# Kernel optimization log

Measured on AMD Instinct MI355X. Metric: run time of the kernel, lower is better.

Reference implementation:

```python
import jax, jax.numpy as jnp
import numpy as np

N = 50000        # nodes
E = 800000       # edges (avg degree 16)
F_IN, F_HID, F_OUT = 128, 256, 256
G = 64           # graphs in batch
NEG_SLOPE_ATT = 0.2   # GATConv attention leaky relu
NEG_SLOPE_ACT = 0.01  # nn.LeakyReLU default


def setup_inputs() -> dict:
    key = jax.random.key(0)
    ks = jax.random.split(key, 12)
    x = jax.random.normal(ks[0], (N, F_IN), dtype=jnp.float32)
    edge_index = jax.random.randint(ks[1], (2, E), 0, N, dtype=jnp.int64)
    batch = jnp.sort(jax.random.randint(ks[2], (N,), 0, G, dtype=jnp.int64))
    def glorot(k, shape):
        fan = sum(shape)
        s = jnp.sqrt(6.0 / fan).astype(jnp.float32)
        return jax.random.uniform(k, shape, jnp.float32, -s, s)
    W1 = glorot(ks[3], (F_IN, F_HID))
    a_s1 = glorot(ks[4], (F_HID,))
    a_d1 = glorot(ks[5], (F_HID,))
    b1 = jnp.zeros((F_HID,), jnp.float32)
    W2 = glorot(ks[6], (F_HID, F_OUT))
    a_s2 = glorot(ks[7], (F_OUT,))
    a_d2 = glorot(ks[8], (F_OUT,))
    b2 = jnp.zeros((F_OUT,), jnp.float32)
    return dict(x=x, edge_index=edge_index, batch=batch,
                W1=W1, a_s1=a_s1, a_d1=a_d1, b1=b1,
                W2=W2, a_s2=a_s2, a_d2=a_d2, b2=b2)


def gat_conv(x, src, dst, W, a_s, a_d, b):
    """Single-head PyG GATConv (self-loops already appended to src/dst)."""
    n = x.shape[0]
    h = x @ W                                   # [N, D]
    alpha_src = h @ a_s                         # [N]
    alpha_dst = h @ a_d                         # [N]
    e = jax.nn.leaky_relu(alpha_src[src] + alpha_dst[dst], NEG_SLOPE_ATT)  # [E+N]
    m = jax.ops.segment_max(e, dst, num_segments=n)
    p = jnp.exp(e - jax.lax.stop_gradient(m)[dst])
    denom = jax.ops.segment_sum(p, dst, num_segments=n)
    alpha = p / denom[dst]                      # softmax over incoming edges
    out = jax.ops.segment_sum(h[src] * alpha[:, None], dst, num_segments=n)
    return out + b


def reference(x, edge_index, batch, W1, a_s1, a_d1, b1, W2, a_s2, a_d2, b2):
    n = x.shape[0]
    loops = jnp.arange(n, dtype=edge_index.dtype)   # GATConv add_self_loops=True
    src = jnp.concatenate([edge_index[0], loops])
    dst = jnp.concatenate([edge_index[1], loops])
    h = gat_conv(x, src, dst, W1, a_s1, a_d1, b1)
    h = jax.nn.leaky_relu(h, NEG_SLOPE_ACT)         # dropout is identity in eval
    node_emb = gat_conv(h, src, dst, W2, a_s2, a_d2, b2)
    graph_emb = jax.ops.segment_sum(node_emb, batch, num_segments=G)
    return node_emb, graph_emb
```

## Files before the change

kernel.cpp:

```cpp
#include <hip/hip_runtime.h>
#include <math.h>

#define NN 50000
#define NE 800000
#define F_IN 128
#define F_HID 256
#define NG 64
#define NPART 8
#define CSR_CHUNKS 128
#define SLOTS 64

typedef __bf16 bf16x8 __attribute__((ext_vector_type(8)));
typedef float f32x4 __attribute__((ext_vector_type(4)));
typedef float f32x2 __attribute__((ext_vector_type(2)));
typedef unsigned short u16x8 __attribute__((ext_vector_type(8)));

static __device__ __forceinline__ unsigned short f2bf(float f) {
    union { float f; unsigned u; } v; v.f = f;
    unsigned r = v.u + 0x7fff + ((v.u >> 16) & 1);
    return (unsigned short)(r >> 16);
}
static __device__ __forceinline__ float bf2f(unsigned short u) {
    union { unsigned u; float f; } v; v.u = ((unsigned)u) << 16;
    return v.f;
}
static __device__ __forceinline__ f32x2 bf2x2(unsigned u) {
    union { unsigned u; float f; } lo, hi;
    lo.u = u << 16;
    hi.u = u & 0xffff0000u;
    f32x2 r; r[0] = lo.f; r[1] = hi.f;
    return r;
}

template <int K, bool AF32, bool ZG>
__global__ __launch_bounds__(256)
void gemm_mfma(const void* __restrict__ Ap, const ushort* __restrict__ Wt,
               ushort* __restrict__ C16, const float* __restrict__ a_s,
               const float* __restrict__ a_d, float* __restrict__ as_out,
               float* __restrict__ ad_out, float* __restrict__ gemb, int M) {
    const ushort* A16 = (const ushort*)Ap;
    const float* A32 = (const float*)Ap;
    __shared__ ushort As[64 * 72];
    __shared__ ushort Bs[256 * 72];
    __shared__ float dps[4][64];
    __shared__ float dpd[4][64];
    const int t = threadIdx.x;
    if (ZG && blockIdx.x < NG) gemb[(size_t)blockIdx.x * 256 + t] = 0.f;
    const int bm = blockIdx.x * 64;
    const int wv = t >> 6, lane = t & 63;
    const int wn = wv * 64;
    const int lrow = lane & 15, quad = lane >> 4;
    const int ar = t >> 2;
    const int ac = (t & 3) << 4;

    f32x4 acc[4][4];
    #pragma unroll
    for (int i = 0; i < 4; ++i)
        #pragma unroll
        for (int j = 0; j < 4; ++j)
            #pragma unroll
            for (int r = 0; r < 4; ++r) acc[i][j][r] = 0.f;

    const int r0 = bm + ar;

    auto load_a = [&](int k0, u16x8& a0, u16x8& a1) {
        a0 = (u16x8)(0); a1 = (u16x8)(0);
        if (r0 < M) {
            if (AF32) {
                const float* p = A32 + (size_t)r0 * K + k0 + ac;
                float4 f0 = *(const float4*)p, f1 = *(const float4*)(p + 4);
                float4 f2 = *(const float4*)(p + 8), f3 = *(const float4*)(p + 12);
                a0[0]=f2bf(f0.x); a0[1]=f2bf(f0.y); a0[2]=f2bf(f0.z); a0[3]=f2bf(f0.w);
                a0[4]=f2bf(f1.x); a0[5]=f2bf(f1.y); a0[6]=f2bf(f1.z); a0[7]=f2bf(f1.w);
                a1[0]=f2bf(f2.x); a1[1]=f2bf(f2.y); a1[2]=f2bf(f2.z); a1[3]=f2bf(f2.w);
                a1[4]=f2bf(f3.x); a1[5]=f2bf(f3.y); a1[6]=f2bf(f3.z); a1[7]=f2bf(f3.w);
            } else {
                const ushort* p = A16 + (size_t)r0 * K + k0 + ac;
                a0 = *(const u16x8*)p;
                a1 = *(const u16x8*)(p + 8);
            }
        }
    };
    auto load_b = [&](int k0, u16x8* b) {
        const ushort* p = Wt + (size_t)t * K + k0;
        #pragma unroll
        for (int j = 0; j < 8; ++j) b[j] = *(const u16x8*)(p + j * 8);
    };

    u16x8 a0, a1, b[8];
    load_a(0, a0, a1);
    load_b(0, b);

    for (int k0 = 0; k0 < K; k0 += 64) {
        __syncthreads();
        *(u16x8*)(As + ar * 72 + ac) = a0;
        *(u16x8*)(As + ar * 72 + ac + 8) = a1;
        #pragma unroll
        for (int j = 0; j < 8; ++j) *(u16x8*)(Bs + t * 72 + j * 8) = b[j];
        __syncthreads();
        bool more = (k0 + 64) < K;
        u16x8 na0, na1, nb[8];
        if (more) {
            load_a(k0 + 64, na0, na1);
            load_b(k0 + 64, nb);
        }
        #pragma unroll
        for (int s = 0; s < 2; ++s) {
            bf16x8 af[4], bf_[4];
            #pragma unroll
            for (int i = 0; i < 4; ++i)
                af[i] = *(const bf16x8*)(As + (i * 16 + lrow) * 72 + s * 32 + quad * 8);
            #pragma unroll
            for (int j = 0; j < 4; ++j)
                bf_[j] = *(const bf16x8*)(Bs + (wn + j * 16 + lrow) * 72 + s * 32 + quad * 8);
            #pragma unroll
            for (int i = 0; i < 4; ++i)
                #pragma unroll
                for (int j = 0; j < 4; ++j)
                    acc[i][j] = __builtin_amdgcn_mfma_f32_16x16x32_bf16(
                        af[i], bf_[j], acc[i][j], 0, 0, 0);
        }
        if (more) {
            a0 = na0; a1 = na1;
            #pragma unroll
            for (int j = 0; j < 8; ++j) b[j] = nb[j];
        }
    }
    float asf[4], adf[4];
    #pragma unroll
    for (int j = 0; j < 4; ++j) {
        asf[j] = a_s[wn + j * 16 + lrow];
        adf[j] = a_d[wn + j * 16 + lrow];
    }
    #pragma unroll
    for (int i = 0; i < 4; ++i) {
        #pragma unroll
        for (int r = 0; r < 4; ++r) {
            float ps = 0.f, pd = 0.f;
            #pragma unroll
            for (int j = 0; j < 4; ++j) {
                ps += acc[i][j][r] * asf[j];
                pd += acc[i][j][r] * adf[j];
            }
            #pragma unroll
            for (int off = 8; off; off >>= 1) {
                ps += __shfl_xor(ps, off);
                pd += __shfl_xor(pd, off);
            }
            if (lrow == 0) {
                dps[wv][i * 16 + quad * 4 + r] = ps;
                dpd[wv][i * 16 + quad * 4 + r] = pd;
            }
        }
    }
    __syncthreads();
    if (t < 64 && bm + t < M) {
        as_out[bm + t] = dps[0][t] + dps[1][t] + dps[2][t] + dps[3][t];
        ad_out[bm + t] = dpd[0][t] + dpd[1][t] + dpd[2][t] + dpd[3][t];
    }
    #pragma unroll
    for (int i = 0; i < 4; ++i) {
        int gm0 = bm + i * 16 + quad * 4;
        #pragma unroll
        for (int j = 0; j < 4; ++j) {
            int gn = wn + j * 16 + lrow;
            #pragma unroll
            for (int r = 0; r < 4; ++r)
                if (gm0 + r < M) C16[(size_t)(gm0 + r) * 256 + gn] = f2bf(acc[i][j][r]);
        }
    }
}

__global__ void cvt_wts(const float* __restrict__ W1, ushort* __restrict__ Wt1,
                        const float* __restrict__ W2, ushort* __restrict__ Wt2,
                        int* __restrict__ cursor) {
    int idx = blockIdx.x * blockDim.x + threadIdx.x;
    if (idx < NN) cursor[idx] = 0;
    if (idx < 256 * F_IN) {
        int n = idx / F_IN, k = idx - n * F_IN;
        Wt1[idx] = f2bf(W1[(size_t)k * 256 + n]);
    } else if (idx < 256 * F_IN + 256 * F_HID) {
        int i2 = idx - 256 * F_IN;
        int n = i2 / F_HID, k = i2 - n * F_HID;
        Wt2[i2] = f2bf(W2[(size_t)k * 256 + n]);
    }
}

__global__ __launch_bounds__(256)
void scatter_part(const int* __restrict__ src, const int* __restrict__ dst,
                  int* __restrict__ cursor, int* __restrict__ src_sorted,
                  int E, int n) {
    const int p = blockIdx.x & (NPART - 1);
    const int c = blockIdx.x >> 3;
    const int T = E + n;
    const int chunk = (T + CSR_CHUNKS - 1) / CSR_CHUNKS;
    const int i0 = c * chunk;
    const int i1 = min(i0 + chunk, T);
    for (int i = i0 + (int)threadIdx.x; i < i1; i += 256) {
        int d = (i < E) ? dst[i] : (i - E);
        int pd = (d * NPART) / NN;
        if (pd == p) {
            int s = (i < E) ? src[i] : d;
            int pos = atomicAdd(&cursor[d], 1);
            if (pos < SLOTS) src_sorted[(size_t)d * SLOTS + pos] = s;
        }
    }
}

template <bool ACT, bool BF16OUT, bool POOL>
__global__ __launch_bounds__(256)
void agg_kernel(const ushort* __restrict__ h, const float* __restrict__ as,
                const float* __restrict__ ad, const int* __restrict__ degs,
                const int* __restrict__ src_sorted, const float* __restrict__ bias,
                float* __restrict__ out, ushort* __restrict__ out16,
                const int* __restrict__ batch, float* __restrict__ gemb, int n) {
    const int hw = threadIdx.x >> 5;
    const int lane = threadIdx.x & 63;
    const int hl = lane & 31;
    const int base = lane & 32;
    const int node = blockIdx.x * 8 + hw;
    __shared__ float vbuf[8][256];
    __shared__ int gids[8];

    const bool valid = node < n;
    int deg = 0, start = 0;
    float adn = 0.f;
    if (valid) {
        deg = min(degs[node], SLOTS);
        start = node * SLOTS;
        adn = ad[node];
    }

    int s_lane = 0;
    float e_lane = -INFINITY;
    if (valid && hl < deg) {
        s_lane = src_sorted[start + hl];
        float e = as[s_lane] + adn;
        e_lane = e > 0.f ? e : 0.2f * e;
    }
    float m = e_lane;
    for (int j = 32 + hl; j < deg; j += 32) {
        int s = src_sorted[start + j];
        float e = as[s] + adn;
        e = e > 0.f ? e : 0.2f * e;
        m = fmaxf(m, e);
    }
    #pragma unroll
    for (int off = 16; off; off >>= 1) m = fmaxf(m, __shfl_xor(m, off));
    float p_lane = __expf(e_lane - m);
    float denom = p_lane;
    for (int j = 32 + hl; j < deg; j += 32) {
        int s = src_sorted[start + j];
        float e = as[s] + adn;
        e = e > 0.f ? e : 0.2f * e;
        denom += __expf(e - m);
    }
    #pragma unroll
    for (int off = 16; off; off >>= 1) denom += __shfl_xor(denom, off);
    float inv = valid ? (1.f / denom) : 0.f;
    p_lane *= inv;

    const ushort* hrow = h + hl * 8;
    f32x2 acc2[4];
    #pragma unroll
    for (int q = 0; q < 4; ++q) { acc2[q][0] = 0.f; acc2[q][1] = 0.f; }
    const int degc = min(deg, 32);
    for (int j0 = 0; j0 < degc; j0 += 4) {
        float wa = __shfl(p_lane, base | j0);       int sa = __shfl(s_lane, base | j0);
        float wb = __shfl(p_lane, base | (j0 + 1)); int sb = __shfl(s_lane, base | (j0 + 1));
        float wc = __shfl(p_lane, base | (j0 + 2)); int sc = __shfl(s_lane, base | (j0 + 2));
        float wd = __shfl(p_lane, base | (j0 + 3)); int sd = __shfl(s_lane, base | (j0 + 3));
        wb = (j0 + 1 < degc) ? wb : 0.f;
        wc = (j0 + 2 < degc) ? wc : 0.f;
        wd = (j0 + 3 < degc) ? wd : 0.f;
        uint4 ra = *(const uint4*)(hrow + (size_t)sa * 256);
        uint4 rb = *(const uint4*)(hrow + (size_t)sb * 256);
        uint4 rc = *(const uint4*)(hrow + (size_t)sc * 256);
        uint4 rd = *(const uint4*)(hrow + (size_t)sd * 256);
        f32x2 wa2; wa2[0] = wa; wa2[1] = wa;
        f32x2 wb2; wb2[0] = wb; wb2[1] = wb;
        f32x2 wc2; wc2[0] = wc; wc2[1] = wc;
        f32x2 wd2; wd2[0] = wd; wd2[1] = wd;
        acc2[0] += wa2 * bf2x2(ra.x); acc2[1] += wa2 * bf2x2(ra.y);
        acc2[2] += wa2 * bf2x2(ra.z); acc2[3] += wa2 * bf2x2(ra.w);
        acc2[0] += wb2 * bf2x2(rb.x); acc2[1] += wb2 * bf2x2(rb.y);
        acc2[2] += wb2 * bf2x2(rb.z); acc2[3] += wb2 * bf2x2(rb.w);
        acc2[0] += wc2 * bf2x2(rc.x); acc2[1] += wc2 * bf2x2(rc.y);
        acc2[2] += wc2 * bf2x2(rc.z); acc2[3] += wc2 * bf2x2(rc.w);
        acc2[0] += wd2 * bf2x2(rd.x); acc2[1] += wd2 * bf2x2(rd.y);
        acc2[2] += wd2 * bf2x2(rd.z); acc2[3] += wd2 * bf2x2(rd.w);
    }
    if (deg > 32) {
        for (int j = 32; j < deg; ++j) {
            int s = src_sorted[start + j];
            float e = as[s] + adn;
            e = e > 0.f ? e : 0.2f * e;
            float w = __expf(e - m) * inv;
            uint4 r = *(const uint4*)(hrow + (size_t)s * 256);
            f32x2 w2; w2[0] = w; w2[1] = w;
            acc2[0] += w2 * bf2x2(r.x); acc2[1] += w2 * bf2x2(r.y);
            acc2[2] += w2 * bf2x2(r.z); acc2[3] += w2 * bf2x2(r.w);
        }
    }
    const float4* b4 = (const float4*)bias;
    float4 b0 = b4[hl * 2], b1 = b4[hl * 2 + 1];
    float v[8];
    v[0] = acc2[0][0] + b0.x; v[1] = acc2[0][1] + b0.y;
    v[2] = acc2[1][0] + b0.z; v[3] = acc2[1][1] + b0.w;
    v[4] = acc2[2][0] + b1.x; v[5] = acc2[2][1] + b1.y;
    v[6] = acc2[3][0] + b1.z; v[7] = acc2[3][1] + b1.w;
    if (ACT) {
        #pragma unroll
        for (int k = 0; k < 8; ++k) v[k] = v[k] > 0.f ? v[k] : 0.01f * v[k];
    }
    if (valid) {
        if (BF16OUT) {
            u16x8 o;
            #pragma unroll
            for (int k = 0; k < 8; ++k) o[k] = f2bf(v[k]);
            *(u16x8*)(out16 + (size_t)node * 256 + hl * 8) = o;
        } else {
            float4 o0 = make_float4(v[0], v[1], v[2], v[3]);
            float4 o1 = make_float4(v[4], v[5], v[6], v[7]);
            float4* op = (float4*)(out + (size_t)node * 256);
            op[hl * 2] = o0;
            op[hl * 2 + 1] = o1;
        }
    }
    if (POOL) {
        *(float4*)&vbuf[hw][hl * 8]     = make_float4(v[0], v[1], v[2], v[3]);
        *(float4*)&vbuf[hw][hl * 8 + 4] = make_float4(v[4], v[5], v[6], v[7]);
        if (hl == 0) gids[hw] = valid ? batch[node] : -1;
        __syncthreads();
        const int t = threadIdx.x;
        float acc = 0.f;
        int cur = gids[0];
        #pragma unroll
        for (int i = 0; i < 8; ++i) {
            int g = gids[i];
            if (g < 0) break;
            if (g != cur) {
                atomicAdd(&gemb[(size_t)cur * 256 + t], acc);
                acc = 0.f; cur = g;
            }
            acc += vbuf[i][t];
        }
        if (cur >= 0) atomicAdd(&gemb[(size_t)cur * 256 + t], acc);
    }
}

static inline char* align_up(char* p, size_t a) {
    return (char*)(((uintptr_t)p + a - 1) & ~(uintptr_t)(a - 1));
}

extern "C" void kernel_launch(void* const* d_in, const int* in_sizes, int n_in,
                              void* d_out, int out_size, void* d_ws, size_t ws_size,
                              hipStream_t stream) {
    const float* x     = (const float*)d_in[0];
    const int* eidx    = (const int*)d_in[1];
    const int* batch   = (const int*)d_in[2];
    const float* W1    = (const float*)d_in[3];
    const float* a_s1  = (const float*)d_in[4];
    const float* a_d1  = (const float*)d_in[5];
    const float* b1    = (const float*)d_in[6];
    const float* W2    = (const float*)d_in[7];
    const float* a_s2  = (const float*)d_in[8];
    const float* a_d2  = (const float*)d_in[9];
    const float* b2    = (const float*)d_in[10];

    float* node_emb  = (float*)d_out;
    float* graph_emb = node_emb + (size_t)NN * 256;

    char* ws = (char*)d_ws;
    ushort* h16  = (ushort*)ws;  ws += (size_t)NN * 256 * sizeof(ushort);
    ws = align_up(ws, 256);
    ushort* z16  = (ushort*)ws;  ws += (size_t)NN * 256 * sizeof(ushort);
    ws = align_up(ws, 256);
    ushort* wt1  = (ushort*)ws;  ws += (size_t)256 * F_IN * sizeof(ushort);
    ws = align_up(ws, 256);
    ushort* wt2  = (ushort*)ws;  ws += (size_t)256 * F_HID * sizeof(ushort);
    ws = align_up(ws, 256);
    float* as_buf = (float*)ws;  ws += (size_t)NN * sizeof(float);
    float* ad_buf = (float*)ws;  ws += (size_t)NN * sizeof(float);
    int* cursor   = (int*)ws;    ws += (size_t)NN * sizeof(int);
    ws = align_up(ws, 256);
    int* src_sorted = (int*)ws;  ws += (size_t)NN * SLOTS * sizeof(int);

    const int* e_src = eidx;
    const int* e_dst = eidx + NE;

    int gemm_blocks = (NN + 63) / 64;
    int agg_blocks = (NN + 7) / 8;

    cvt_wts<<<(256 * (F_IN + F_HID) + 255) / 256, 256, 0, stream>>>(W1, wt1, W2, wt2, cursor);

    scatter_part<<<NPART * CSR_CHUNKS, 256, 0, stream>>>(e_src, e_dst, cursor, src_sorted, NE, NN);

    gemm_mfma<F_IN, true, false><<<gemm_blocks, 256, 0, stream>>>(
        x, wt1, h16, a_s1, a_d1, as_buf, ad_buf, nullptr, NN);
    agg_kernel<true, true, false><<<agg_blocks, 256, 0, stream>>>(
        h16, as_buf, ad_buf, cursor, src_sorted, b1, nullptr, z16, nullptr, nullptr, NN);

    gemm_mfma<F_HID, false, true><<<gemm_blocks, 256, 0, stream>>>(
        z16, wt2, h16, a_s2, a_d2, as_buf, ad_buf, graph_emb, NN);
    agg_kernel<false, false, true><<<agg_blocks, 256, 0, stream>>>(
        h16, as_buf, ad_buf, cursor, src_sorted, b2, node_emb, nullptr, batch, graph_emb, NN);
}
```

Measured before the change: 316.2 us.

## Quantize node features to int8 with per-row scales for aggregation gathers

The GEMM epilogue now computes a per-row absmax, stores a scale per node, and writes the transformed features as int8 instead of bf16. The aggregation kernels gather 8-byte int8 rows and fold the scale into the attention weight, halving gather traffic over the roughly 850K edges. The cost is an extra reduction and barrier in the GEMM epilogue, byte-granular scattered stores, more integer-to-float conversion work per gathered element, and reduced numerical precision that may exceed tolerance.

```diff
diff --git a/kernel.cpp b/kernel.cpp
--- a/kernel.cpp
+++ b/kernel.cpp
@@ -12,7 +12,6 @@
 
 typedef __bf16 bf16x8 __attribute__((ext_vector_type(8)));
 typedef float f32x4 __attribute__((ext_vector_type(4)));
-typedef float f32x2 __attribute__((ext_vector_type(2)));
 typedef unsigned short u16x8 __attribute__((ext_vector_type(8)));
 
 static __device__ __forceinline__ unsigned short f2bf(float f) {
@@ -20,30 +19,30 @@
     unsigned r = v.u + 0x7fff + ((v.u >> 16) & 1);
     return (unsigned short)(r >> 16);
 }
-static __device__ __forceinline__ float bf2f(unsigned short u) {
-    union { unsigned u; float f; } v; v.u = ((unsigned)u) << 16;
-    return v.f;
-}
-static __device__ __forceinline__ f32x2 bf2x2(unsigned u) {
-    union { unsigned u; float f; } lo, hi;
-    lo.u = u << 16;
-    hi.u = u & 0xffff0000u;
-    f32x2 r; r[0] = lo.f; r[1] = hi.f;
-    return r;
+static __device__ __forceinline__ void i8fma(float* acc8, unsigned lo, unsigned hi, float w) {
+    #pragma unroll
+    for (int k = 0; k < 4; ++k)
+        acc8[k]     += w * (float)(int)(signed char)(lo >> (k * 8));
+    #pragma unroll
+    for (int k = 0; k < 4; ++k)
+        acc8[k + 4] += w * (float)(int)(signed char)(hi >> (k * 8));
 }
 
 template <int K, bool AF32, bool ZG>
 __global__ __launch_bounds__(256)
 void gemm_mfma(const void* __restrict__ Ap, const ushort* __restrict__ Wt,
-               ushort* __restrict__ C16, const float* __restrict__ a_s,
-               const float* __restrict__ a_d, float* __restrict__ as_out,
-               float* __restrict__ ad_out, float* __restrict__ gemb, int M) {
+               signed char* __restrict__ C8, float* __restrict__ scales,
+               const float* __restrict__ a_s, const float* __restrict__ a_d,
+               float* __restrict__ as_out, float* __restrict__ ad_out,
+               float* __restrict__ gemb, int M) {
     const ushort* A16 = (const ushort*)Ap;
     const float* A32 = (const float*)Ap;
     __shared__ ushort As[64 * 72];
     __shared__ ushort Bs[256 * 72];
     __shared__ float dps[4][64];
     __shared__ float dpd[4][64];
+    __shared__ float rmx[4][64];
+    __shared__ float rinvs[64];
     const int t = threadIdx.x;
     if (ZG && blockIdx.x < NG) gemb[(size_t)blockIdx.x * 256 + t] = 0.f;
     const int bm = blockIdx.x * 64;
@@ -136,37 +135,53 @@
     for (int i = 0; i < 4; ++i) {
         #pragma unroll
         for (int r = 0; r < 4; ++r) {
-            float ps = 0.f, pd = 0.f;
+            float ps = 0.f, pd = 0.f, mx = 0.f;
             #pragma unroll
             for (int j = 0; j < 4; ++j) {
                 ps += acc[i][j][r] * asf[j];
                 pd += acc[i][j][r] * adf[j];
+                mx = fmaxf(mx, fabsf(acc[i][j][r]));
             }
             #pragma unroll
             for (int off = 8; off; off >>= 1) {
                 ps += __shfl_xor(ps, off);
                 pd += __shfl_xor(pd, off);
+                mx = fmaxf(mx, __shfl_xor(mx, off));
             }
             if (lrow == 0) {
                 dps[wv][i * 16 + quad * 4 + r] = ps;
                 dpd[wv][i * 16 + quad * 4 + r] = pd;
+                rmx[wv][i * 16 + quad * 4 + r] = mx;
             }
         }
     }
     __syncthreads();
-    if (t < 64 && bm + t < M) {
-        as_out[bm + t] = dps[0][t] + dps[1][t] + dps[2][t] + dps[3][t];
-        ad_out[bm + t] = dpd[0][t] + dpd[1][t] + dpd[2][t] + dpd[3][t];
-    }
+    if (t < 64) {
+        float mx = fmaxf(fmaxf(rmx[0][t], rmx[1][t]), fmaxf(rmx[2][t], rmx[3][t]));
+        rinvs[t] = mx > 0.f ? 127.f / mx : 0.f;
+        if (bm + t < M) {
+            scales[bm + t] = mx * (1.f / 127.f);
+            as_out[bm + t] = dps[0][t] + dps[1][t] + dps[2][t] + dps[3][t];
+            ad_out[bm + t] = dpd[0][t] + dpd[1][t] + dpd[2][t] + dpd[3][t];
+        }
+    }
+    __syncthreads();
     #pragma unroll
     for (int i = 0; i < 4; ++i) {
-        int gm0 = bm + i * 16 + quad * 4;
-        #pragma unroll
-        for (int j = 0; j < 4; ++j) {
-            int gn = wn + j * 16 + lrow;
-            #pragma unroll
-            for (int r = 0; r < 4; ++r)
-                if (gm0 + r < M) C16[(size_t)(gm0 + r) * 256 + gn] = f2bf(acc[i][j][r]);
+        #pragma unroll
+        for (int r = 0; r < 4; ++r) {
+            int rl = i * 16 + quad * 4 + r;
+            int gm = bm + rl;
+            if (gm < M) {
+                float rinv = rinvs[rl];
+                #pragma unroll
+                for (int j = 0; j < 4; ++j) {
+                    int gn = wn + j * 16 + lrow;
+                    int qi = __float2int_rn(acc[i][j][r] * rinv);
+                    qi = max(-127, min(127, qi));
+                    C8[(size_t)gm * 256 + gn] = (signed char)qi;
+                }
+            }
         }
     }
 }
@@ -209,11 +224,12 @@
 
 template <bool ACT, bool BF16OUT, bool POOL>
 __global__ __launch_bounds__(256)
-void agg_kernel(const ushort* __restrict__ h, const float* __restrict__ as,
-                const float* __restrict__ ad, const int* __restrict__ degs,
-                const int* __restrict__ src_sorted, const float* __restrict__ bias,
-                float* __restrict__ out, ushort* __restrict__ out16,
-                const int* __restrict__ batch, float* __restrict__ gemb, int n) {
+void agg_kernel(const signed char* __restrict__ h8, const float* __restrict__ scales,
+                const float* __restrict__ as, const float* __restrict__ ad,
+                const int* __restrict__ degs, const int* __restrict__ src_sorted,
+                const float* __restrict__ bias, float* __restrict__ out,
+                ushort* __restrict__ out16, const int* __restrict__ batch,
+                float* __restrict__ gemb, int n) {
     const int hw = threadIdx.x >> 5;
     const int lane = threadIdx.x & 63;
     const int hl = lane & 31;
@@ -232,11 +248,12 @@
     }
 
     int s_lane = 0;
-    float e_lane = -INFINITY;
+    float e_lane = -INFINITY, sc_lane = 0.f;
     if (valid && hl < deg) {
         s_lane = src_sorted[start + hl];
         float e = as[s_lane] + adn;
         e_lane = e > 0.f ? e : 0.2f * e;
+        sc_lane = scales[s_lane];
     }
     float m = e_lane;
     for (int j = 32 + hl; j < deg; j += 32) {
@@ -258,57 +275,45 @@
     #pragma unroll
     for (int off = 16; off; off >>= 1) denom += __shfl_xor(denom, off);
     float inv = valid ? (1.f / denom) : 0.f;
-    p_lane *= inv;
-
-    const ushort* hrow = h + hl * 8;
-    f32x2 acc2[4];
-    #pragma unroll
-    for (int q = 0; q < 4; ++q) { acc2[q][0] = 0.f; acc2[q][1] = 0.f; }
+    float q_lane = p_lane * inv * sc_lane;
+
+    const signed char* hrow = h8 + hl * 8;
+    float acc8[8] = {0.f, 0.f, 0.f, 0.f, 0.f, 0.f, 0.f, 0.f};
     const int degc = min(deg, 32);
     for (int j0 = 0; j0 < degc; j0 += 4) {
-        float wa = __shfl(p_lane, base | j0);       int sa = __shfl(s_lane, base | j0);
-        float wb = __shfl(p_lane, base | (j0 + 1)); int sb = __shfl(s_lane, base | (j0 + 1));
-        float wc = __shfl(p_lane, base | (j0 + 2)); int sc = __shfl(s_lane, base | (j0 + 2));
-        float wd = __shfl(p_lane, base | (j0 + 3)); int sd = __shfl(s_lane, base | (j0 + 3));
+        float wa = __shfl(q_lane, base | j0);       int sa = __shfl(s_lane, base | j0);
+        float wb = __shfl(q_lane, base | (j0 + 1)); int sb = __shfl(s_lane, base | (j0 + 1));
+        float wc = __shfl(q_lane, base | (j0 + 2)); int sc = __shfl(s_lane, base | (j0 + 2));
+        float wd = __shfl(q_lane, base | (j0 + 3)); int sd = __shfl(s_lane, base | (j0 + 3));
         wb = (j0 + 1 < degc) ? wb : 0.f;
         wc = (j0 + 2 < degc) ? wc : 0.f;
         wd = (j0 + 3 < degc) ? wd : 0.f;
-        uint4 ra = *(const uint4*)(hrow + (size_t)sa * 256);
-        uint4 rb = *(const uint4*)(hrow + (size_t)sb * 256);
-        uint4 rc = *(const uint4*)(hrow + (size_t)sc * 256);
-        uint4 rd = *(const uint4*)(hrow + (size_t)sd * 256);
-        f32x2 wa2; wa2[0] = wa; wa2[1] = wa;
-        f32x2 wb2; wb2[0] = wb; wb2[1] = wb;
-        f32x2 wc2; wc2[0] = wc; wc2[1] = wc;
-        f32x2 wd2; wd2[0] = wd; wd2[1] = wd;
-        acc2[0] += wa2 * bf2x2(ra.x); acc2[1] += wa2 * bf2x2(ra.y);
-        acc2[2] += wa2 * bf2x2(ra.z); acc2[3] += wa2 * bf2x2(ra.w);
-        acc2[0] += wb2 * bf2x2(rb.x); acc2[1] += wb2 * bf2x2(rb.y);
-        acc2[2] += wb2 * bf2x2(rb.z); acc2[3] += wb2 * bf2x2(rb.w);
-        acc2[0] += wc2 * bf2x2(rc.x); acc2[1] += wc2 * bf2x2(rc.y);
-        acc2[2] += wc2 * bf2x2(rc.z); acc2[3] += wc2 * bf2x2(rc.w);
-        acc2[0] += wd2 * bf2x2(rd.x); acc2[1] += wd2 * bf2x2(rd.y);
-        acc2[2] += wd2 * bf2x2(rd.z); acc2[3] += wd2 * bf2x2(rd.w);
+        uint2 ra = *(const uint2*)(hrow + (size_t)sa * 256);
+        uint2 rb = *(const uint2*)(hrow + (size_t)sb * 256);
+        uint2 rc = *(const uint2*)(hrow + (size_t)sc * 256);
+        uint2 rd = *(const uint2*)(hrow + (size_t)sd * 256);
+        i8fma(acc8, ra.x, ra.y, wa);
+        i8fma(acc8, rb.x, rb.y, wb);
+        i8fma(acc8, rc.x, rc.y, wc);
+        i8fma(acc8, rd.x, rd.y, wd);
     }
     if (deg > 32) {
         for (int j = 32; j < deg; ++j) {
             int s = src_sorted[start + j];
             float e = as[s] + adn;
             e = e > 0.f ? e : 0.2f * e;
-            float w = __expf(e - m) * inv;
-            uint4 r = *(const uint4*)(hrow + (size_t)s * 256);
-            f32x2 w2; w2[0] = w; w2[1] = w;
-            acc2[0] += w2 * bf2x2(r.x); acc2[1] += w2 * bf2x2(r.y);
-            acc2[2] += w2 * bf2x2(r.z); acc2[3] += w2 * bf2x2(r.w);
+            float w = __expf(e - m) * inv * scales[s];
+            uint2 r = *(const uint2*)(hrow + (size_t)s * 256);
+            i8fma(acc8, r.x, r.y, w);
         }
     }
     const float4* b4 = (const float4*)bias;
     float4 b0 = b4[hl * 2], b1 = b4[hl * 2 + 1];
     float v[8];
-    v[0] = acc2[0][0] + b0.x; v[1] = acc2[0][1] + b0.y;
-    v[2] = acc2[1][0] + b0.z; v[3] = acc2[1][1] + b0.w;
-    v[4] = acc2[2][0] + b1.x; v[5] = acc2[2][1] + b1.y;
-    v[6] = acc2[3][0] + b1.z; v[7] = acc2[3][1] + b1.w;
+    v[0] = acc8[0] + b0.x; v[1] = acc8[1] + b0.y;
+    v[2] = acc8[2] + b0.z; v[3] = acc8[3] + b0.w;
+    v[4] = acc8[4] + b1.x; v[5] = acc8[5] + b1.y;
+    v[6] = acc8[6] + b1.z; v[7] = acc8[7] + b1.w;
     if (ACT) {
         #pragma unroll
         for (int k = 0; k < 8; ++k) v[k] = v[k] > 0.f ? v[k] : 0.01f * v[k];
@@ -372,7 +377,9 @@
     float* graph_emb = node_emb + (size_t)NN * 256;
 
     char* ws = (char*)d_ws;
-    ushort* h16  = (ushort*)ws;  ws += (size_t)NN * 256 * sizeof(ushort);
+    signed char* h8 = (signed char*)ws; ws += (size_t)NN * 256;
+    ws = align_up(ws, 256);
+    float* scl   = (float*)ws;   ws += (size_t)NN * sizeof(float);
     ws = align_up(ws, 256);
     ushort* z16  = (ushort*)ws;  ws += (size_t)NN * 256 * sizeof(ushort);
     ws = align_up(ws, 256);
@@ -397,12 +404,12 @@
     scatter_part<<<NPART * CSR_CHUNKS, 256, 0, stream>>>(e_src, e_dst, cursor, src_sorted, NE, NN);
 
     gemm_mfma<F_IN, true, false><<<gemm_blocks, 256, 0, stream>>>(
-        x, wt1, h16, a_s1, a_d1, as_buf, ad_buf, nullptr, NN);
+        x, wt1, h8, scl, a_s1, a_d1, as_buf, ad_buf, nullptr, NN);
     agg_kernel<true, true, false><<<agg_blocks, 256, 0, stream>>>(
-        h16, as_buf, ad_buf, cursor, src_sorted, b1, nullptr, z16, nullptr, nullptr, NN);
+        h8, scl, as_buf, ad_buf, cursor, src_sorted, b1, nullptr, z16, nullptr, nullptr, NN);
 
     gemm_mfma<F_HID, false, true><<<gemm_blocks, 256, 0, stream>>>(
-        z16, wt2, h16, a_s2, a_d2, as_buf, ad_buf, graph_emb, NN);
+        z16, wt2, h8, scl, a_s2, a_d2, as_buf, ad_buf, graph_emb, NN);
     agg_kernel<false, false, true><<<agg_blocks, 256, 0, stream>>>(
-        h16, as_buf, ad_buf, cursor, src_sorted, b2, node_emb, nullptr, batch, graph_emb, NN);
-}
+        h8, scl, as_buf, ad_buf, cursor, src_sorted, b2, node_emb, nullptr, batch, graph_emb, NN);
+}
```

Measured after the change: 271.7 us. 1.16x faster.
